# Optimization experiments

Measured on AMD Instinct MI355X. Metric: run time of the kernel, lower is better.

## Reference

```python
import jax, jax.numpy as jnp
import numpy as np

B, T, E, H = 4, 2048, 1024, 1024

def setup_inputs() -> dict:
    key = jax.random.key(0)
    k1, k2, k3, k4 = jax.random.split(key, 4)
    inputs = jax.random.normal(k1, (B, T, E), dtype=jnp.float32)
    # Dense(size, use_bias=False) -> weight [emb, size], glorot-ish scale
    Wq = jax.random.normal(k2, (E, H), dtype=jnp.float32) * (1.0 / np.sqrt(E))
    Wk = jax.random.normal(k3, (E, H), dtype=jnp.float32) * (1.0 / np.sqrt(E))
    Wv = jax.random.normal(k4, (E, H), dtype=jnp.float32) * (1.0 / np.sqrt(E))
    return {"inputs": inputs, "Wq": Wq, "Wk": Wk, "Wv": Wv}

def reference(inputs, Wq, Wk, Wv):
    # inputs: [B, T, E]
    _, Tc, Ec = inputs.shape
    q = inputs @ Wq  # [B, T, H]
    k = inputs @ Wk  # [B, T, H]
    v = inputs @ Wv  # [B, T, H]
    # scores scaled by emb_dim**-0.5 (NOT head size) as in the source
    w = jnp.einsum('bih,bjh->bij', q, k) * (Ec ** -0.5)  # [B, T, T]
    tril = jnp.tril(jnp.ones((Tc, Tc), dtype=bool))
    w = jnp.where(tril, w, -jnp.inf)
    # NOTE: source uses softmax over axis=1 (query axis), non-standard but faithful
    w = jax.nn.softmax(w, axis=1)
    # dropout_rate=0.0 -> identity
    out = w @ v  # [B, T, H]
    return out
```

## Files before the change

kernel.cpp:

```cpp
#include <hip/hip_runtime.h>
#include <hip/hip_bf16.h>
#include <stdint.h>


typedef short bf16x8 __attribute__((ext_vector_type(8)));
typedef float f32x4  __attribute__((ext_vector_type(4)));

__device__ __forceinline__ unsigned short f2bf(float f) {
    union { float f; unsigned u; } x; x.f = f;
    unsigned r = x.u + 0x7FFFu + ((x.u >> 16) & 1u);
    return (unsigned short)(r >> 16);
}
__device__ __forceinline__ float bf2f(unsigned short h) {
    union { unsigned u; float f; } x; x.u = ((unsigned)h) << 16;
    return x.f;
}

__global__ __launch_bounds__(256) void prep_kernel(
    const float* __restrict__ X,
    const float* __restrict__ Wq, const float* __restrict__ Wk,
    const float* __restrict__ Wv,
    unsigned short* __restrict__ Xb, unsigned short* __restrict__ WT)
{
    __shared__ unsigned short tile[64][65];
    unsigned id = blockIdx.x;
    if (id < 8192) {
        size_t i = ((size_t)id * 256 + threadIdx.x) * 4;
        float4 v = *(const float4*)(X + i);
        union { unsigned short h[4]; unsigned long long u; } p;
        p.h[0] = f2bf(v.x); p.h[1] = f2bf(v.y);
        p.h[2] = f2bf(v.z); p.h[3] = f2bf(v.w);
        *(unsigned long long*)(Xb + i) = p.u;
    } else {
        unsigned w = id - 8192;
        unsigned which = w >> 8;
        const float* W = (which == 0) ? Wq : (which == 1) ? Wk : Wv;
        unsigned short* out = WT + (size_t)which * 1024 * 1024;
        const int R = 1024, C = 1024;
        unsigned t2 = w & 255;
        int c0 = (int)(t2 & 15) * 64, r0 = (int)(t2 >> 4) * 64;
        int tx = threadIdx.x & 63, ty = threadIdx.x >> 6;
#pragma unroll
        for (int i = 0; i < 16; ++i) {
            int r = ty + i * 4;
            tile[r][tx] = f2bf(W[(size_t)(r0 + r) * C + c0 + tx]);
        }
        __syncthreads();
#pragma unroll
        for (int i = 0; i < 16; ++i) {
            int c = ty + i * 4;
            out[(size_t)(c0 + c) * R + r0 + tx] = tile[tx][c];
        }
    }
}

__global__ __launch_bounds__(256, 3) void gemm_nt_qkv(
    const unsigned short* __restrict__ A, const unsigned short* __restrict__ B,
    unsigned short* __restrict__ Cout, unsigned short* __restrict__ C2,
    unsigned short* __restrict__ C3, int K, int ldt, int tmoff)
{
    unsigned id = blockIdx.y * gridDim.x + blockIdx.x;
    unsigned xcd = id & 7, k2 = id >> 3;
    int tm = (int)(xcd * 4 + (k2 & 3)) + tmoff;
    int tn = (int)(k2 >> 2);
    int m0 = tm * 128, n0 = tn * 128;
    int kmax = K;

    __shared__ unsigned short sAB[2 * 128 * 64];
    char* sAc = (char*)sAB;
    char* sBc = (char*)sAB + 16384;

    unsigned t = threadIdx.x, lane = t & 63, wave = t >> 6;

    unsigned srow = t >> 2;
    unsigned gsw = (t & 3) ^ ((t >> 3) & 3);
    const unsigned short* pA = A + (size_t)(m0 + srow) * K + gsw * 8;
    const unsigned short* pB = B + (size_t)(n0 + srow) * K + gsw * 8;
    const size_t rstep = (size_t)64 * K;
    unsigned ldsOff = t * 16;

    unsigned wm = (wave >> 1) * 64, wn = (wave & 1) * 64;
    unsigned lrow = lane & 15;
    unsigned lk = ((lane >> 4) ^ ((lane >> 1) & 3)) * 8;
    const short* sAs = (const short*)sAB;
    const short* sBs = (const short*)(sAB + 128 * 64);

    f32x4 acc[4][4] = {};

    int4 rA0 = *(const int4*)(pA);
    int4 rA1 = *(const int4*)(pA + rstep);
    int4 rA2 = *(const int4*)(pA + 32);
    int4 rA3 = *(const int4*)(pA + rstep + 32);
    int4 rB0 = *(const int4*)(pB);
    int4 rB1 = *(const int4*)(pB + rstep);
    int4 rB2 = *(const int4*)(pB + 32);
    int4 rB3 = *(const int4*)(pB + rstep + 32);

    for (int k0 = 0; k0 < kmax; k0 += 64) {
        __syncthreads();
        *(int4*)(sAc + ldsOff)         = rA0;
        *(int4*)(sAc + ldsOff + 4096)  = rA1;
        *(int4*)(sAc + ldsOff + 8192)  = rA2;
        *(int4*)(sAc + ldsOff + 12288) = rA3;
        *(int4*)(sBc + ldsOff)         = rB0;
        *(int4*)(sBc + ldsOff + 4096)  = rB1;
        *(int4*)(sBc + ldsOff + 8192)  = rB2;
        *(int4*)(sBc + ldsOff + 12288) = rB3;
        __syncthreads();

        if (k0 + 64 < kmax) {
            pA += 64; pB += 64;
            rA0 = *(const int4*)(pA);
            rA1 = *(const int4*)(pA + rstep);
            rA2 = *(const int4*)(pA + 32);
            rA3 = *(const int4*)(pA + rstep + 32);
            rB0 = *(const int4*)(pB);
            rB1 = *(const int4*)(pB + rstep);
            rB2 = *(const int4*)(pB + 32);
            rB3 = *(const int4*)(pB + rstep + 32);
        }

#pragma unroll
        for (int kk = 0; kk < 2; ++kk) {
            bf16x8 a[4], b[4];
#pragma unroll
            for (int i = 0; i < 4; ++i) {
                a[i] = *(const bf16x8*)(sAs + kk * 4096 + (wm + i * 16 + lrow) * 32 + lk);
                b[i] = *(const bf16x8*)(sBs + kk * 4096 + (wn + i * 16 + lrow) * 32 + lk);
            }
#pragma unroll
            for (int i = 0; i < 4; ++i)
#pragma unroll
                for (int j = 0; j < 4; ++j)
                    acc[i][j] = __builtin_amdgcn_mfma_f32_16x16x32_bf16(
                        a[i], b[j], acc[i][j], 0, 0, 0);
        }
    }

    unsigned col = lane & 15, rq = (lane >> 4) * 4;
    if (n0 < 2048) {
        unsigned short* C = (n0 < 1024) ? Cout : C2;
        int nb = n0 & 1023;
#pragma unroll
        for (int i = 0; i < 4; ++i)
#pragma unroll
            for (int j = 0; j < 4; ++j)
#pragma unroll
                for (int r = 0; r < 4; ++r)
                    C[(size_t)(m0 + wm + i * 16 + rq + r) * 1024 + nb + wn + j * 16 + col] =
                        f2bf(acc[i][j][r]);
    } else {
        int batch = m0 >> 11, tb = m0 & 2047;
        unsigned short* C = C3 + (size_t)batch * 1024 * 2048;
#pragma unroll
        for (int i = 0; i < 4; ++i)
#pragma unroll
            for (int j = 0; j < 4; ++j) {
                union { unsigned short h[4]; unsigned long long u; } p;
#pragma unroll
                for (int r = 0; r < 4; ++r) p.h[r] = f2bf(acc[i][j][r]);
                int h = (n0 - 2048) + wn + j * 16 + col;
                int t0 = tb + wm + i * 16 + rq;
                *(unsigned long long*)(C + (size_t)h * ldt + t0) = p.u;
            }
    }
}

__global__ __launch_bounds__(256, 4) void scores64_kernel(
    const unsigned short* __restrict__ A, const unsigned short* __restrict__ B,
    unsigned short* __restrict__ Eb, float* __restrict__ fpar, float scale)
{
    int bz = blockIdx.z;
    unsigned bx = blockIdx.x;
    int u = (int)((bx & 7u) * 34u + (bx >> 3));
    int tm = (int)((sqrtf(4.f * (float)u + 1.f) - 1.f) * 0.5f);
    while ((tm + 1) * (tm + 2) <= u) ++tm;
    while (tm * (tm + 1) > u) --tm;
    int tn64 = u - tm * (tm + 1);
    const int K = 1024;
    int m0 = tm * 128, n0 = tn64 * 64;
    A += (size_t)bz * (size_t)2048 * 1024;
    B += (size_t)bz * (size_t)2048 * 1024;

    __shared__ unsigned short sAB[12288];
    char* sAc = (char*)sAB;
    char* sBc = (char*)sAB + 16384;

    unsigned t = threadIdx.x, lane = t & 63, wave = t >> 6;
    unsigned srow = t >> 2;
    unsigned gsw = (t & 3) ^ ((t >> 3) & 3);
    const unsigned short* pA = A + (size_t)(m0 + srow) * K + gsw * 8;
    const unsigned short* pB = B + (size_t)(n0 + srow) * K + gsw * 8;
    const size_t rstep = (size_t)64 * K;
    unsigned ldsOff = t * 16;

    unsigned wm = (wave >> 1) * 64, wn = (wave & 1) * 32;
    unsigned lrow = lane & 15;
    unsigned lk = ((lane >> 4) ^ ((lane >> 1) & 3)) * 8;
    const short* sAs = (const short*)sAB;
    const short* sBs = (const short*)(sAB + 8192);

    f32x4 acc[4][2] = {};

    int4 rA0 = *(const int4*)(pA);
    int4 rA1 = *(const int4*)(pA + rstep);
    int4 rA2 = *(const int4*)(pA + 32);
    int4 rA3 = *(const int4*)(pA + rstep + 32);
    int4 rB0 = *(const int4*)(pB);
    int4 rB1 = *(const int4*)(pB + 32);

    for (int k0 = 0; k0 < K; k0 += 64) {
        __syncthreads();
        *(int4*)(sAc + ldsOff)         = rA0;
        *(int4*)(sAc + ldsOff + 4096)  = rA1;
        *(int4*)(sAc + ldsOff + 8192)  = rA2;
        *(int4*)(sAc + ldsOff + 12288) = rA3;
        *(int4*)(sBc + ldsOff)         = rB0;
        *(int4*)(sBc + ldsOff + 4096)  = rB1;
        __syncthreads();

        if (k0 + 64 < K) {
            pA += 64; pB += 64;
            rA0 = *(const int4*)(pA);
            rA1 = *(const int4*)(pA + rstep);
            rA2 = *(const int4*)(pA + 32);
            rA3 = *(const int4*)(pA + rstep + 32);
            rB0 = *(const int4*)(pB);
            rB1 = *(const int4*)(pB + 32);
        }

#pragma unroll
        for (int kk = 0; kk < 2; ++kk) {
            bf16x8 a[4], b[2];
#pragma unroll
            for (int i = 0; i < 4; ++i)
                a[i] = *(const bf16x8*)(sAs + kk * 4096 + (wm + i * 16 + lrow) * 32 + lk);
#pragma unroll
            for (int j = 0; j < 2; ++j)
                b[j] = *(const bf16x8*)(sBs + kk * 2048 + (wn + j * 16 + lrow) * 32 + lk);
#pragma unroll
            for (int i = 0; i < 4; ++i)
#pragma unroll
                for (int j = 0; j < 2; ++j)
                    acc[i][j] = __builtin_amdgcn_mfma_f32_16x16x32_bf16(
                        a[i], b[j], acc[i][j], 0, 0, 0);
        }
    }

    unsigned col = lane & 15, rq = (lane >> 4) * 4;
    unsigned short* Ebp = Eb + (size_t)bz * (size_t)2048 * 2048;
    float* par = fpar + (size_t)bz * 32 * 2048;
    bool diag = ((tn64 >> 1) == tm);
    unsigned short* tile = sAB;
    __syncthreads();
#pragma unroll
    for (int jj = 0; jj < 2; ++jj) {
        float csum = 0.f;
        int jl = (int)(wn + jj * 16 + col);
        int jg = n0 + jl;
#pragma unroll
        for (int ii = 0; ii < 4; ++ii) {
#pragma unroll
            for (int r = 0; r < 4; ++r) {
                int il = (int)(wm + ii * 16 + rq + r);
                int ig = m0 + il;
                unsigned short us = 0;
                if (!diag || ig >= jg)
                    us = f2bf(__expf(acc[ii][jj][r] * scale));
                tile[il * 64 + jl] = us;
                csum += bf2f(us);
            }
        }
        csum += __shfl_xor(csum, 16);
        csum += __shfl_xor(csum, 32);
        if (lane < 16) {
            int rh = (m0 + (int)wm) >> 6;
            par[(size_t)rh * 2048 + n0 + wn + jj * 16 + lane] = csum;
        }
    }
    __syncthreads();
    {
        unsigned rr = t >> 3, cc = (t & 7) * 8;
#pragma unroll
        for (int p = 0; p < 4; ++p) {
            int li = (int)(p * 32 + rr);
            int4 v = *(const int4*)(tile + li * 64 + cc);
            *(int4*)(Ebp + (size_t)(m0 + li) * 2048 + n0 + cc) = v;
        }
    }
}

__global__ __launch_bounds__(256, 3) void pv128_kernel(
    const unsigned short* __restrict__ A, const unsigned short* __restrict__ B,
    float* __restrict__ out)
{
    unsigned n = blockIdx.x;
    int tn = (int)(n & 7u);
    unsigned q = n >> 3, half = q >> 5, r = q & 31u;
    int bz = (int)((half ? 2u : 0u) + (r & 1u));
    int tm = half ? (int)(r >> 1) : (int)(15u - (r >> 1));
    const int K = 2048, N = 1024;
    int m0 = tm * 128, n0 = tn * 128;
    int kmax = m0 + 128;
    A += (size_t)bz * (size_t)2048 * 2048;
    B += (size_t)bz * (size_t)1024 * 2048;

    __shared__ unsigned short sAB[2 * 128 * 64];
    char* sAc = (char*)sAB;
    char* sBc = (char*)sAB + 16384;

    unsigned t = threadIdx.x, lane = t & 63, wave = t >> 6;

    unsigned srow = t >> 2;
    unsigned gsw = (t & 3) ^ ((t >> 3) & 3);
    const unsigned short* pA = A + (size_t)(m0 + srow) * K + gsw * 8;
    const unsigned short* pB = B + (size_t)(n0 + srow) * K + gsw * 8;
    const size_t rstep = (size_t)64 * K;
    unsigned ldsOff = t * 16;

    unsigned wm = (wave >> 1) * 64, wn = (wave & 1) * 64;
    unsigned lrow = lane & 15;
    unsigned lk = ((lane >> 4) ^ ((lane >> 1) & 3)) * 8;
    const short* sAs = (const short*)sAB;
    const short* sBs = (const short*)(sAB + 128 * 64);

    f32x4 acc[4][4] = {};

    int4 rA0 = *(const int4*)(pA);
    int4 rA1 = *(const int4*)(pA + rstep);
    int4 rA2 = *(const int4*)(pA + 32);
    int4 rA3 = *(const int4*)(pA + rstep + 32);
    int4 rB0 = *(const int4*)(pB);
    int4 rB1 = *(const int4*)(pB + rstep);
    int4 rB2 = *(const int4*)(pB + 32);
    int4 rB3 = *(const int4*)(pB + rstep + 32);

    for (int k0 = 0; k0 < kmax; k0 += 64) {
        __syncthreads();
        *(int4*)(sAc + ldsOff)         = rA0;
        *(int4*)(sAc + ldsOff + 4096)  = rA1;
        *(int4*)(sAc + ldsOff + 8192)  = rA2;
        *(int4*)(sAc + ldsOff + 12288) = rA3;
        *(int4*)(sBc + ldsOff)         = rB0;
        *(int4*)(sBc + ldsOff + 4096)  = rB1;
        *(int4*)(sBc + ldsOff + 8192)  = rB2;
        *(int4*)(sBc + ldsOff + 12288) = rB3;
        __syncthreads();

        if (k0 + 64 < kmax) {
            pA += 64; pB += 64;
            rA0 = *(const int4*)(pA);
            rA1 = *(const int4*)(pA + rstep);
            rA2 = *(const int4*)(pA + 32);
            rA3 = *(const int4*)(pA + rstep + 32);
            rB0 = *(const int4*)(pB);
            rB1 = *(const int4*)(pB + rstep);
            rB2 = *(const int4*)(pB + 32);
            rB3 = *(const int4*)(pB + rstep + 32);
        }

#pragma unroll
        for (int kk = 0; kk < 2; ++kk) {
            bf16x8 a[4], b[4];
#pragma unroll
            for (int i = 0; i < 4; ++i) {
                a[i] = *(const bf16x8*)(sAs + kk * 4096 + (wm + i * 16 + lrow) * 32 + lk);
                b[i] = *(const bf16x8*)(sBs + kk * 4096 + (wn + i * 16 + lrow) * 32 + lk);
            }
#pragma unroll
            for (int i = 0; i < 4; ++i)
#pragma unroll
                for (int j = 0; j < 4; ++j)
                    acc[i][j] = __builtin_amdgcn_mfma_f32_16x16x32_bf16(
                        a[i], b[j], acc[i][j], 0, 0, 0);
        }
    }

    unsigned col = lane & 15, rq = (lane >> 4) * 4;
    float* C = out + (size_t)bz * (size_t)2048 * 1024;
#pragma unroll
    for (int i = 0; i < 4; ++i)
#pragma unroll
        for (int j = 0; j < 4; ++j)
#pragma unroll
            for (int r = 0; r < 4; ++r)
                C[(size_t)(m0 + wm + i * 16 + rq + r) * N + n0 + wn + j * 16 + col] =
                    acc[i][j][r];
}

__global__ __launch_bounds__(256) void colsum_scale(
    const float* __restrict__ par, unsigned short* __restrict__ Vt)
{
    int b = blockIdx.z, t0 = blockIdx.x * 64, h0 = blockIdx.y * 128;
    __shared__ float Ls[64];
    int tid = threadIdx.x;
    if (tid < 64) {
        int j = t0 + tid;
        const float* p = par + (size_t)b * 32 * 2048;
        float s = 0.f;
        for (int rh = j >> 6; rh < 32; ++rh) s += p[(size_t)rh * 2048 + j];
        Ls[tid] = 1.0f / s;
    }
    __syncthreads();
    unsigned short* V = Vt + ((size_t)b << 21);
    int c8 = (tid & 7) * 8;
#pragma unroll
    for (int rr = 0; rr < 4; ++rr) {
        int h = h0 + rr * 32 + (tid >> 3);
        size_t idx = (size_t)h * 2048 + t0 + c8;
        bf16x8 v = *(bf16x8*)(V + idx);
#pragma unroll
        for (int e = 0; e < 8; ++e)
            v[e] = (short)f2bf(bf2f((unsigned short)v[e]) * Ls[c8 + e]);
        *(bf16x8*)(V + idx) = v;
    }
}

extern "C" void kernel_launch(void* const* d_in, const int* in_sizes, int n_in,
                              void* d_out, int out_size, void* d_ws, size_t ws_size,
                              hipStream_t stream)
{
    const int B = 4, T = 2048, E = 1024, H = 1024;
    const int M = B * T;
    const float* X  = (const float*)d_in[0];
    const float* Wq = (const float*)d_in[1];
    const float* Wk = (const float*)d_in[2];
    const float* Wv = (const float*)d_in[3];
    float* out = (float*)d_out;
    char* ws = (char*)d_ws;
    const size_t MB = 1024 * 1024;

    unsigned short* Xb  = (unsigned short*)(ws + 0);
    unsigned short* WqT = (unsigned short*)(ws + 16 * MB);
    unsigned short* Qb  = (unsigned short*)(ws + 32 * MB);
    unsigned short* Kb  = (unsigned short*)(ws + 48 * MB);
    unsigned short* Vt  = (unsigned short*)(ws + 64 * MB);
    unsigned short* Eb  = (unsigned short*)(ws + 0);
    float*          par  = (float*)d_out;

    prep_kernel<<<dim3(8960), 256, 0, stream>>>(X, Wq, Wk, Wv, Xb, WqT);

    gemm_nt_qkv<<<dim3(24, 32, 1), 256, 0, stream>>>(
        Xb, WqT, Qb, Kb, Vt, E, T, 0);
    gemm_nt_qkv<<<dim3(24, 32, 1), 256, 0, stream>>>(
        Xb, WqT, Qb, Kb, Vt, E, T, 32);

    scores64_kernel<<<dim3(272, 1, B), 256, 0, stream>>>(
        Qb, Kb, Eb, par, 0.03125f);

    colsum_scale<<<dim3(32, 8, 4), 256, 0, stream>>>(par, Vt);

    pv128_kernel<<<dim3(512), 256, 0, stream>>>(Eb, Vt, out);
}
```

Before: 235.3 us.

## Fuse fp32-to-bf16 conversion of X into QKV GEMM and merge launches

Removes the separate X conversion pass from the prep kernel. The QKV GEMM now loads fp32 X directly and packs it to bf16 when writing to shared memory, which saves writing and re-reading a 16MB bf16 copy. The two half-grid GEMM launches are merged into one launch with a remapped tile index. The trade-off is that the GEMM's A-operand global reads double in bytes, and each re-read of X across the 24 column tiles now fetches fp32 instead of bf16, adding register and bandwidth pressure.

```diff
diff --git a/kernel.cpp b/kernel.cpp
--- a/kernel.cpp
+++ b/kernel.cpp
@@ -15,54 +15,48 @@
     union { unsigned u; float f; } x; x.u = ((unsigned)h) << 16;
     return x.f;
 }
+__device__ __forceinline__ int4 pack8(float4 a, float4 b) {
+    union { unsigned short h[8]; int4 v; } p;
+    p.h[0] = f2bf(a.x); p.h[1] = f2bf(a.y); p.h[2] = f2bf(a.z); p.h[3] = f2bf(a.w);
+    p.h[4] = f2bf(b.x); p.h[5] = f2bf(b.y); p.h[6] = f2bf(b.z); p.h[7] = f2bf(b.w);
+    return p.v;
+}
 
 __global__ __launch_bounds__(256) void prep_kernel(
-    const float* __restrict__ X,
     const float* __restrict__ Wq, const float* __restrict__ Wk,
-    const float* __restrict__ Wv,
-    unsigned short* __restrict__ Xb, unsigned short* __restrict__ WT)
+    const float* __restrict__ Wv, unsigned short* __restrict__ WT)
 {
     __shared__ unsigned short tile[64][65];
-    unsigned id = blockIdx.x;
-    if (id < 8192) {
-        size_t i = ((size_t)id * 256 + threadIdx.x) * 4;
-        float4 v = *(const float4*)(X + i);
-        union { unsigned short h[4]; unsigned long long u; } p;
-        p.h[0] = f2bf(v.x); p.h[1] = f2bf(v.y);
-        p.h[2] = f2bf(v.z); p.h[3] = f2bf(v.w);
-        *(unsigned long long*)(Xb + i) = p.u;
-    } else {
-        unsigned w = id - 8192;
-        unsigned which = w >> 8;
-        const float* W = (which == 0) ? Wq : (which == 1) ? Wk : Wv;
-        unsigned short* out = WT + (size_t)which * 1024 * 1024;
-        const int R = 1024, C = 1024;
-        unsigned t2 = w & 255;
-        int c0 = (int)(t2 & 15) * 64, r0 = (int)(t2 >> 4) * 64;
-        int tx = threadIdx.x & 63, ty = threadIdx.x >> 6;
-#pragma unroll
-        for (int i = 0; i < 16; ++i) {
-            int r = ty + i * 4;
-            tile[r][tx] = f2bf(W[(size_t)(r0 + r) * C + c0 + tx]);
-        }
-        __syncthreads();
-#pragma unroll
-        for (int i = 0; i < 16; ++i) {
-            int c = ty + i * 4;
-            out[(size_t)(c0 + c) * R + r0 + tx] = tile[tx][c];
-        }
+    unsigned w = blockIdx.x;
+    unsigned which = w >> 8;
+    const float* W = (which == 0) ? Wq : (which == 1) ? Wk : Wv;
+    unsigned short* out = WT + (size_t)which * 1024 * 1024;
+    const int R = 1024, C = 1024;
+    unsigned t2 = w & 255;
+    int c0 = (int)(t2 & 15) * 64, r0 = (int)(t2 >> 4) * 64;
+    int tx = threadIdx.x & 63, ty = threadIdx.x >> 6;
+#pragma unroll
+    for (int i = 0; i < 16; ++i) {
+        int r = ty + i * 4;
+        tile[r][tx] = f2bf(W[(size_t)(r0 + r) * C + c0 + tx]);
+    }
+    __syncthreads();
+#pragma unroll
+    for (int i = 0; i < 16; ++i) {
+        int c = ty + i * 4;
+        out[(size_t)(c0 + c) * R + r0 + tx] = tile[tx][c];
     }
 }
 
 __global__ __launch_bounds__(256, 3) void gemm_nt_qkv(
-    const unsigned short* __restrict__ A, const unsigned short* __restrict__ B,
+    const float* __restrict__ X, const unsigned short* __restrict__ B,
     unsigned short* __restrict__ Cout, unsigned short* __restrict__ C2,
-    unsigned short* __restrict__ C3, int K, int ldt, int tmoff)
+    unsigned short* __restrict__ C3, int K, int ldt)
 {
     unsigned id = blockIdx.y * gridDim.x + blockIdx.x;
     unsigned xcd = id & 7, k2 = id >> 3;
-    int tm = (int)(xcd * 4 + (k2 & 3)) + tmoff;
-    int tn = (int)(k2 >> 2);
+    int tm = (int)(xcd * 8 + (k2 & 7));
+    int tn = (int)(k2 >> 3);
     int m0 = tm * 128, n0 = tn * 128;
     int kmax = K;
 
@@ -74,7 +68,7 @@
 
     unsigned srow = t >> 2;
     unsigned gsw = (t & 3) ^ ((t >> 3) & 3);
-    const unsigned short* pA = A + (size_t)(m0 + srow) * K + gsw * 8;
+    const float* pA = X + (size_t)(m0 + srow) * K + gsw * 8;
     const unsigned short* pB = B + (size_t)(n0 + srow) * K + gsw * 8;
     const size_t rstep = (size_t)64 * K;
     unsigned ldsOff = t * 16;
@@ -87,10 +81,14 @@
 
     f32x4 acc[4][4] = {};
 
-    int4 rA0 = *(const int4*)(pA);
-    int4 rA1 = *(const int4*)(pA + rstep);
-    int4 rA2 = *(const int4*)(pA + 32);
-    int4 rA3 = *(const int4*)(pA + rstep + 32);
+    float4 fA0a = *(const float4*)(pA);
+    float4 fA0b = *(const float4*)(pA + 4);
+    float4 fA1a = *(const float4*)(pA + rstep);
+    float4 fA1b = *(const float4*)(pA + rstep + 4);
+    float4 fA2a = *(const float4*)(pA + 32);
+    float4 fA2b = *(const float4*)(pA + 36);
+    float4 fA3a = *(const float4*)(pA + rstep + 32);
+    float4 fA3b = *(const float4*)(pA + rstep + 36);
     int4 rB0 = *(const int4*)(pB);
     int4 rB1 = *(const int4*)(pB + rstep);
     int4 rB2 = *(const int4*)(pB + 32);
@@ -98,10 +96,10 @@
 
     for (int k0 = 0; k0 < kmax; k0 += 64) {
         __syncthreads();
-        *(int4*)(sAc + ldsOff)         = rA0;
-        *(int4*)(sAc + ldsOff + 4096)  = rA1;
-        *(int4*)(sAc + ldsOff + 8192)  = rA2;
-        *(int4*)(sAc + ldsOff + 12288) = rA3;
+        *(int4*)(sAc + ldsOff)         = pack8(fA0a, fA0b);
+        *(int4*)(sAc + ldsOff + 4096)  = pack8(fA1a, fA1b);
+        *(int4*)(sAc + ldsOff + 8192)  = pack8(fA2a, fA2b);
+        *(int4*)(sAc + ldsOff + 12288) = pack8(fA3a, fA3b);
         *(int4*)(sBc + ldsOff)         = rB0;
         *(int4*)(sBc + ldsOff + 4096)  = rB1;
         *(int4*)(sBc + ldsOff + 8192)  = rB2;
@@ -110,10 +108,14 @@
 
         if (k0 + 64 < kmax) {
             pA += 64; pB += 64;
-            rA0 = *(const int4*)(pA);
-            rA1 = *(const int4*)(pA + rstep);
-            rA2 = *(const int4*)(pA + 32);
-            rA3 = *(const int4*)(pA + rstep + 32);
+            fA0a = *(const float4*)(pA);
+            fA0b = *(const float4*)(pA + 4);
+            fA1a = *(const float4*)(pA + rstep);
+            fA1b = *(const float4*)(pA + rstep + 4);
+            fA2a = *(const float4*)(pA + 32);
+            fA2b = *(const float4*)(pA + 36);
+            fA3a = *(const float4*)(pA + rstep + 32);
+            fA3b = *(const float4*)(pA + rstep + 36);
             rB0 = *(const int4*)(pB);
             rB1 = *(const int4*)(pB + rstep);
             rB2 = *(const int4*)(pB + 32);
@@ -430,7 +432,6 @@
     char* ws = (char*)d_ws;
     const size_t MB = 1024 * 1024;
 
-    unsigned short* Xb  = (unsigned short*)(ws + 0);
     unsigned short* WqT = (unsigned short*)(ws + 16 * MB);
     unsigned short* Qb  = (unsigned short*)(ws + 32 * MB);
     unsigned short* Kb  = (unsigned short*)(ws + 48 * MB);
@@ -438,12 +439,10 @@
     unsigned short* Eb  = (unsigned short*)(ws + 0);
     float*          par  = (float*)d_out;
 
-    prep_kernel<<<dim3(8960), 256, 0, stream>>>(X, Wq, Wk, Wv, Xb, WqT);
-
-    gemm_nt_qkv<<<dim3(24, 32, 1), 256, 0, stream>>>(
-        Xb, WqT, Qb, Kb, Vt, E, T, 0);
-    gemm_nt_qkv<<<dim3(24, 32, 1), 256, 0, stream>>>(
-        Xb, WqT, Qb, Kb, Vt, E, T, 32);
+    prep_kernel<<<dim3(768), 256, 0, stream>>>(Wq, Wk, Wv, WqT);
+
+    gemm_nt_qkv<<<dim3(24, 64, 1), 256, 0, stream>>>(
+        X, WqT, Qb, Kb, Vt, E, T);
 
     scores64_kernel<<<dim3(272, 1, B), 256, 0, stream>>>(
         Qb, Kb, Eb, par, 0.03125f);
```

Result: no change. 231.1 us (-1.8%).

## Fuse column-sum scaling of V into PV GEMM and merge QKV GEMM launches

Applied to the files above, without the earlier changes.

Replaces the colsum_scale kernel, which read, scaled and rewrote all of Vt, with a small colsum_inv kernel that only writes per-column inverse sums. The PV GEMM now loads those inverses and scales the V tile as it stores it to LDS. This removes a full read-modify-write pass over V at the cost of extra ALU work inside the GEMM loop. The two half-grid QKV GEMM launches are also merged into one launch with a remapped tile index, removing one launch and its tail. Linv reuses the Q buffer region, which is safe only because Q is dead once the scores kernel has run.

```diff
diff --git a/kernel.cpp b/kernel.cpp
--- a/kernel.cpp
+++ b/kernel.cpp
@@ -14,6 +14,18 @@
 __device__ __forceinline__ float bf2f(unsigned short h) {
     union { unsigned u; float f; } x; x.u = ((unsigned)h) << 16;
     return x.f;
+}
+__device__ __forceinline__ int4 scale8(int4 v, float4 l0, float4 l1) {
+    union { unsigned short h[8]; int4 v; } p; p.v = v;
+    p.h[0] = f2bf(bf2f(p.h[0]) * l0.x);
+    p.h[1] = f2bf(bf2f(p.h[1]) * l0.y);
+    p.h[2] = f2bf(bf2f(p.h[2]) * l0.z);
+    p.h[3] = f2bf(bf2f(p.h[3]) * l0.w);
+    p.h[4] = f2bf(bf2f(p.h[4]) * l1.x);
+    p.h[5] = f2bf(bf2f(p.h[5]) * l1.y);
+    p.h[6] = f2bf(bf2f(p.h[6]) * l1.z);
+    p.h[7] = f2bf(bf2f(p.h[7]) * l1.w);
+    return p.v;
 }
 
 __global__ __launch_bounds__(256) void prep_kernel(
@@ -57,12 +69,12 @@
 __global__ __launch_bounds__(256, 3) void gemm_nt_qkv(
     const unsigned short* __restrict__ A, const unsigned short* __restrict__ B,
     unsigned short* __restrict__ Cout, unsigned short* __restrict__ C2,
-    unsigned short* __restrict__ C3, int K, int ldt, int tmoff)
+    unsigned short* __restrict__ C3, int K, int ldt)
 {
     unsigned id = blockIdx.y * gridDim.x + blockIdx.x;
     unsigned xcd = id & 7, k2 = id >> 3;
-    int tm = (int)(xcd * 4 + (k2 & 3)) + tmoff;
-    int tn = (int)(k2 >> 2);
+    int tm = (int)(xcd * 8 + (k2 & 7));
+    int tn = (int)(k2 >> 3);
     int m0 = tm * 128, n0 = tn * 128;
     int kmax = K;
 
@@ -290,9 +302,20 @@
     }
 }
 
+__global__ __launch_bounds__(256) void colsum_inv(
+    const float* __restrict__ par, float* __restrict__ Linv)
+{
+    int b = blockIdx.y;
+    int j = blockIdx.x * 256 + threadIdx.x;
+    const float* p = par + (size_t)b * 32 * 2048;
+    float s = 0.f;
+    for (int rh = j >> 6; rh < 32; ++rh) s += p[(size_t)rh * 2048 + j];
+    Linv[b * 2048 + j] = 1.0f / s;
+}
+
 __global__ __launch_bounds__(256, 3) void pv128_kernel(
     const unsigned short* __restrict__ A, const unsigned short* __restrict__ B,
-    float* __restrict__ out)
+    const float* __restrict__ LinvG, float* __restrict__ out)
 {
     unsigned n = blockIdx.x;
     int tn = (int)(n & 7u);
@@ -304,6 +327,7 @@
     int kmax = m0 + 128;
     A += (size_t)bz * (size_t)2048 * 2048;
     B += (size_t)bz * (size_t)1024 * 2048;
+    const float* Lv = LinvG + bz * 2048;
 
     __shared__ unsigned short sAB[2 * 128 * 64];
     char* sAc = (char*)sAB;
@@ -313,8 +337,9 @@
 
     unsigned srow = t >> 2;
     unsigned gsw = (t & 3) ^ ((t >> 3) & 3);
-    const unsigned short* pA = A + (size_t)(m0 + srow) * K + gsw * 8;
-    const unsigned short* pB = B + (size_t)(n0 + srow) * K + gsw * 8;
+    unsigned g8 = gsw * 8;
+    const unsigned short* pA = A + (size_t)(m0 + srow) * K + g8;
+    const unsigned short* pB = B + (size_t)(n0 + srow) * K + g8;
     const size_t rstep = (size_t)64 * K;
     unsigned ldsOff = t * 16;
 
@@ -334,6 +359,10 @@
     int4 rB1 = *(const int4*)(pB + rstep);
     int4 rB2 = *(const int4*)(pB + 32);
     int4 rB3 = *(const int4*)(pB + rstep + 32);
+    float4 L0a = *(const float4*)(Lv + g8);
+    float4 L0b = *(const float4*)(Lv + g8 + 4);
+    float4 L1a = *(const float4*)(Lv + g8 + 32);
+    float4 L1b = *(const float4*)(Lv + g8 + 36);
 
     for (int k0 = 0; k0 < kmax; k0 += 64) {
         __syncthreads();
@@ -341,10 +370,10 @@
         *(int4*)(sAc + ldsOff + 4096)  = rA1;
         *(int4*)(sAc + ldsOff + 8192)  = rA2;
         *(int4*)(sAc + ldsOff + 12288) = rA3;
-        *(int4*)(sBc + ldsOff)         = rB0;
-        *(int4*)(sBc + ldsOff + 4096)  = rB1;
-        *(int4*)(sBc + ldsOff + 8192)  = rB2;
-        *(int4*)(sBc + ldsOff + 12288) = rB3;
+        *(int4*)(sBc + ldsOff)         = scale8(rB0, L0a, L0b);
+        *(int4*)(sBc + ldsOff + 4096)  = scale8(rB1, L0a, L0b);
+        *(int4*)(sBc + ldsOff + 8192)  = scale8(rB2, L1a, L1b);
+        *(int4*)(sBc + ldsOff + 12288) = scale8(rB3, L1a, L1b);
         __syncthreads();
 
         if (k0 + 64 < kmax) {
@@ -357,6 +386,11 @@
             rB1 = *(const int4*)(pB + rstep);
             rB2 = *(const int4*)(pB + 32);
             rB3 = *(const int4*)(pB + rstep + 32);
+            const float* Lk = Lv + k0 + 64 + g8;
+            L0a = *(const float4*)(Lk);
+            L0b = *(const float4*)(Lk + 4);
+            L1a = *(const float4*)(Lk + 32);
+            L1b = *(const float4*)(Lk + 36);
         }
 
 #pragma unroll
@@ -386,34 +420,6 @@
             for (int r = 0; r < 4; ++r)
                 C[(size_t)(m0 + wm + i * 16 + rq + r) * N + n0 + wn + j * 16 + col] =
                     acc[i][j][r];
-}
-
-__global__ __launch_bounds__(256) void colsum_scale(
-    const float* __restrict__ par, unsigned short* __restrict__ Vt)
-{
-    int b = blockIdx.z, t0 = blockIdx.x * 64, h0 = blockIdx.y * 128;
-    __shared__ float Ls[64];
-    int tid = threadIdx.x;
-    if (tid < 64) {
-        int j = t0 + tid;
-        const float* p = par + (size_t)b * 32 * 2048;
-        float s = 0.f;
-        for (int rh = j >> 6; rh < 32; ++rh) s += p[(size_t)rh * 2048 + j];
-        Ls[tid] = 1.0f / s;
-    }
-    __syncthreads();
-    unsigned short* V = Vt + ((size_t)b << 21);
-    int c8 = (tid & 7) * 8;
-#pragma unroll
-    for (int rr = 0; rr < 4; ++rr) {
-        int h = h0 + rr * 32 + (tid >> 3);
-        size_t idx = (size_t)h * 2048 + t0 + c8;
-        bf16x8 v = *(bf16x8*)(V + idx);
-#pragma unroll
-        for (int e = 0; e < 8; ++e)
-            v[e] = (short)f2bf(bf2f((unsigned short)v[e]) * Ls[c8 + e]);
-        *(bf16x8*)(V + idx) = v;
-    }
 }
 
 extern "C" void kernel_launch(void* const* d_in, const int* in_sizes, int n_in,
@@ -436,19 +442,18 @@
     unsigned short* Kb  = (unsigned short*)(ws + 48 * MB);
     unsigned short* Vt  = (unsigned short*)(ws + 64 * MB);
     unsigned short* Eb  = (unsigned short*)(ws + 0);
+    float*          Linv = (float*)(ws + 32 * MB);
     float*          par  = (float*)d_out;
 
     prep_kernel<<<dim3(8960), 256, 0, stream>>>(X, Wq, Wk, Wv, Xb, WqT);
 
-    gemm_nt_qkv<<<dim3(24, 32, 1), 256, 0, stream>>>(
-        Xb, WqT, Qb, Kb, Vt, E, T, 0);
-    gemm_nt_qkv<<<dim3(24, 32, 1), 256, 0, stream>>>(
-        Xb, WqT, Qb, Kb, Vt, E, T, 32);
+    gemm_nt_qkv<<<dim3(24, 64, 1), 256, 0, stream>>>(
+        Xb, WqT, Qb, Kb, Vt, E, T);
 
     scores64_kernel<<<dim3(272, 1, B), 256, 0, stream>>>(
         Qb, Kb, Eb, par, 0.03125f);
 
-    colsum_scale<<<dim3(32, 8, 4), 256, 0, stream>>>(par, Vt);
-
-    pv128_kernel<<<dim3(512), 256, 0, stream>>>(Eb, Vt, out);
-}
+    colsum_inv<<<dim3(T / 256, B), 256, 0, stream>>>(par, Linv);
+
+    pv128_kernel<<<dim3(512), 256, 0, stream>>>(Eb, Vt, Linv, out);
+}
```

Result: no change. 234.3 us (-0.4%).

## Load QKV GEMM tiles directly into LDS and merge the two launches

Applied to the files above, without the earlier changes.

The QKV projection GEMM now uses global_load_lds to copy A and B tiles straight from global memory into shared memory, replacing the register-staged prefetch and the separate LDS stores. The LDS layout changes to a plain row-major 64-wide k layout without the XOR swizzle. The two half-grid launches are merged into one launch of double height, with a new tile mapping. The software prefetch overlap is gone, because loads are now issued and waited on within each iteration, and the unswizzled layout may cause LDS bank conflicts on the MFMA operand reads.

```diff
diff --git a/kernel.cpp b/kernel.cpp
--- a/kernel.cpp
+++ b/kernel.cpp
@@ -15,6 +15,11 @@
     union { unsigned u; float f; } x; x.u = ((unsigned)h) << 16;
     return x.f;
 }
+
+#define GLOAD16(gp, lp) \
+    __builtin_amdgcn_global_load_lds( \
+        (const __attribute__((address_space(1))) unsigned int*)(gp), \
+        (__attribute__((address_space(3))) unsigned int*)(lp), 16, 0, 0)
 
 __global__ __launch_bounds__(256) void prep_kernel(
     const float* __restrict__ X,
@@ -57,76 +62,53 @@
 __global__ __launch_bounds__(256, 3) void gemm_nt_qkv(
     const unsigned short* __restrict__ A, const unsigned short* __restrict__ B,
     unsigned short* __restrict__ Cout, unsigned short* __restrict__ C2,
-    unsigned short* __restrict__ C3, int K, int ldt, int tmoff)
+    unsigned short* __restrict__ C3, int K, int ldt)
 {
     unsigned id = blockIdx.y * gridDim.x + blockIdx.x;
     unsigned xcd = id & 7, k2 = id >> 3;
-    int tm = (int)(xcd * 4 + (k2 & 3)) + tmoff;
-    int tn = (int)(k2 >> 2);
+    int tm = (int)(xcd * 8 + (k2 & 7));
+    int tn = (int)(k2 >> 3);
     int m0 = tm * 128, n0 = tn * 128;
-    int kmax = K;
-
-    __shared__ unsigned short sAB[2 * 128 * 64];
-    char* sAc = (char*)sAB;
-    char* sBc = (char*)sAB + 16384;
+
+    __shared__ __align__(128) unsigned short sAB[2 * 128 * 64];
 
     unsigned t = threadIdx.x, lane = t & 63, wave = t >> 6;
 
-    unsigned srow = t >> 2;
-    unsigned gsw = (t & 3) ^ ((t >> 3) & 3);
-    const unsigned short* pA = A + (size_t)(m0 + srow) * K + gsw * 8;
-    const unsigned short* pB = B + (size_t)(n0 + srow) * K + gsw * 8;
-    const size_t rstep = (size_t)64 * K;
-    unsigned ldsOff = t * 16;
+    unsigned srow = t >> 3;
+    unsigned kc = t & 7;
+    const unsigned short* pA = A + (size_t)(m0 + srow) * K + kc * 8;
+    const unsigned short* pB = B + (size_t)(n0 + srow) * K + kc * 8;
+    const size_t r32 = (size_t)32 * K;
+    char* ldsw = (char*)sAB + wave * 1024;
 
     unsigned wm = (wave >> 1) * 64, wn = (wave & 1) * 64;
     unsigned lrow = lane & 15;
-    unsigned lk = ((lane >> 4) ^ ((lane >> 1) & 3)) * 8;
+    unsigned lk = (lane >> 4) * 8;
     const short* sAs = (const short*)sAB;
     const short* sBs = (const short*)(sAB + 128 * 64);
 
     f32x4 acc[4][4] = {};
 
-    int4 rA0 = *(const int4*)(pA);
-    int4 rA1 = *(const int4*)(pA + rstep);
-    int4 rA2 = *(const int4*)(pA + 32);
-    int4 rA3 = *(const int4*)(pA + rstep + 32);
-    int4 rB0 = *(const int4*)(pB);
-    int4 rB1 = *(const int4*)(pB + rstep);
-    int4 rB2 = *(const int4*)(pB + 32);
-    int4 rB3 = *(const int4*)(pB + rstep + 32);
-
-    for (int k0 = 0; k0 < kmax; k0 += 64) {
-        __syncthreads();
-        *(int4*)(sAc + ldsOff)         = rA0;
-        *(int4*)(sAc + ldsOff + 4096)  = rA1;
-        *(int4*)(sAc + ldsOff + 8192)  = rA2;
-        *(int4*)(sAc + ldsOff + 12288) = rA3;
-        *(int4*)(sBc + ldsOff)         = rB0;
-        *(int4*)(sBc + ldsOff + 4096)  = rB1;
-        *(int4*)(sBc + ldsOff + 8192)  = rB2;
-        *(int4*)(sBc + ldsOff + 12288) = rB3;
-        __syncthreads();
-
-        if (k0 + 64 < kmax) {
-            pA += 64; pB += 64;
-            rA0 = *(const int4*)(pA);
-            rA1 = *(const int4*)(pA + rstep);
-            rA2 = *(const int4*)(pA + 32);
-            rA3 = *(const int4*)(pA + rstep + 32);
-            rB0 = *(const int4*)(pB);
-            rB1 = *(const int4*)(pB + rstep);
-            rB2 = *(const int4*)(pB + 32);
-            rB3 = *(const int4*)(pB + rstep + 32);
-        }
+    for (int k0 = 0; k0 < K; k0 += 64) {
+        __syncthreads();
+        GLOAD16(pA,           ldsw);
+        GLOAD16(pA +     r32, ldsw + 4096);
+        GLOAD16(pA + 2 * r32, ldsw + 8192);
+        GLOAD16(pA + 3 * r32, ldsw + 12288);
+        GLOAD16(pB,           ldsw + 16384);
+        GLOAD16(pB +     r32, ldsw + 20480);
+        GLOAD16(pB + 2 * r32, ldsw + 24576);
+        GLOAD16(pB + 3 * r32, ldsw + 28672);
+        pA += 64; pB += 64;
+        __syncthreads();
 
 #pragma unroll
         for (int kk = 0; kk < 2; ++kk) {
             bf16x8 a[4], b[4];
 #pragma unroll
             for (int i = 0; i < 4; ++i) {
-                a[i] = *(const bf16x8*)(sAs + kk * 4096 + (wm + i * 16 + lrow) * 32 + lk);
-                b[i] = *(const bf16x8*)(sBs + kk * 4096 + (wn + i * 16 + lrow) * 32 + lk);
+                a[i] = *(const bf16x8*)(sAs + (wm + i * 16 + lrow) * 64 + kk * 32 + lk);
+                b[i] = *(const bf16x8*)(sBs + (wn + i * 16 + lrow) * 64 + kk * 32 + lk);
             }
 #pragma unroll
             for (int i = 0; i < 4; ++i)
@@ -440,10 +422,8 @@
 
     prep_kernel<<<dim3(8960), 256, 0, stream>>>(X, Wq, Wk, Wv, Xb, WqT);
 
-    gemm_nt_qkv<<<dim3(24, 32, 1), 256, 0, stream>>>(
-        Xb, WqT, Qb, Kb, Vt, E, T, 0);
-    gemm_nt_qkv<<<dim3(24, 32, 1), 256, 0, stream>>>(
-        Xb, WqT, Qb, Kb, Vt, E, T, 32);
+    gemm_nt_qkv<<<dim3(24, 64, 1), 256, 0, stream>>>(
+        Xb, WqT, Qb, Kb, Vt, E, T);
 
     scores64_kernel<<<dim3(272, 1, B), 256, 0, stream>>>(
         Qb, Kb, Eb, par, 0.03125f);
```

Measured after the change: 228.9 us. 1.03x faster.
